# Optimization experiments

Measured on AMD Instinct MI355X. Metric: run time of the kernel, lower is better.

The kernel has to match this reference:

```python
import jax, jax.numpy as jnp
import numpy as np

N_NODES = 100000
N_EDGES = 1600000
D_IN, D_HID, D_OUT = 128, 64, 64


def setup_inputs() -> dict:
    key = jax.random.key(0)
    k0, k1, k2, k3 = jax.random.split(key, 4)
    X = jax.random.normal(k0, (N_NODES, D_IN), dtype=jnp.float32)
    E = jax.random.randint(k1, (2, N_EDGES), 0, N_NODES, dtype=jnp.int32)
    W1 = jax.random.normal(k2, (D_IN, D_HID), dtype=jnp.float32) * 0.05
    b1 = jnp.zeros((D_HID,), dtype=jnp.float32)
    W2 = jax.random.normal(k3, (D_HID, D_OUT), dtype=jnp.float32) * 0.05
    b2 = jnp.zeros((D_OUT,), dtype=jnp.float32)
    return {"V": N_NODES, "E": E, "X": X, "W1": W1, "b1": b1, "W2": W2, "b2": b2}


def _gcn_layer(X, W, b, src, dst, norm, n):
    # GCNConv: linear transform (no bias), gather, degree-normalize, scatter-add, + bias
    Xl = X @ W                              # [n, d_out]
    msg = Xl[src] * norm[:, None]           # [n_edges_sl, d_out] gather
    out = jax.ops.segment_sum(msg, dst, num_segments=n)  # scatter-add
    return out + b


def reference(V, E, X, W1, b1, W2, b2):
    n = X.shape[0]
    # add self loops (add_self_loops=True)
    loop = jnp.arange(n, dtype=E.dtype)
    src = jnp.concatenate([E[0], loop])
    dst = jnp.concatenate([E[1], loop])
    # symmetric gcn_norm: deg over target nodes (unit edge weights)
    deg = jax.ops.segment_sum(jnp.ones_like(dst, dtype=X.dtype), dst, num_segments=n)
    dinv = jnp.where(deg > 0, jax.lax.rsqrt(deg), 0.0)
    norm = dinv[src] * dinv[dst]
    H = jax.nn.relu(_gcn_layer(X, W1, b1, src, dst, norm, n))
    # last layer: no ReLU (matches torch module)
    return _gcn_layer(H, W2, b2, src, dst, norm, n)
```

## Files before the change

### kernel.cpp

```cpp
#include <hip/hip_runtime.h>

#define NT 256
#define TILE 256
#define TILE_SH 8
#define BSTRIDE 8192
#define BSTRIDE_SH 13
#define EPB 4096
#define ITB 16
#define NBUCK_PAD 512

static inline int cdiv(long long a, long long b) { return (int)((a + b - 1) / b); }

typedef unsigned int uint32;
typedef unsigned short ushort16;
typedef short bf16x8 __attribute__((ext_vector_type(8)));
typedef float f32x4 __attribute__((ext_vector_type(4)));

__device__ __forceinline__ ushort16 f2bf(float f) {
  uint32 u = __float_as_uint(f);
  u = (u + 0x7FFF + ((u >> 16) & 1)) >> 16;
  return (ushort16)u;
}
__device__ __forceinline__ float bflo(uint32 w) { return __uint_as_float(w << 16); }
__device__ __forceinline__ float bfhi(uint32 w) { return __uint_as_float(w & 0xFFFF0000u); }
__device__ __forceinline__ float bf2f(ushort16 h) { return __uint_as_float(((uint32)h) << 16); }

template <int K, int BFIN, int SPLIT>
__device__ __forceinline__ void gemm_body(const void* __restrict__ Xp,
                                          const float* __restrict__ W,
                                          uint2* __restrict__ Yb, int n, int base,
                                          unsigned short* Xh, unsigned short* XlA,
                                          unsigned short* Wt) {
  constexpr int STR = K + 8;
  const int tid = threadIdx.x;

  for (int i = tid; i < K * 64; i += NT) {
    int k = i >> 6, nn = i & 63;
    Wt[nn * STR + k] = f2bf(W[i]);
  }
  if (BFIN) {
    constexpr int NU = K / 8;
    const uint4* X4 = (const uint4*)Xp;
    for (int i = tid; i < 64 * NU; i += NT) {
      int row = i / NU, u = i % NU;
      int v = base + row;
      uint4 val = make_uint4(0u, 0u, 0u, 0u);
      if (v < n) val = X4[(size_t)v * NU + u];
      *(uint4*)&Xh[row * STR + u * 8] = val;
    }
  } else {
    constexpr int KQ = K / 4;
    const float4* X4 = (const float4*)Xp;
    for (int i = tid; i < 64 * KQ; i += NT) {
      int row = i / KQ, q = i % KQ;
      int v = base + row;
      float4 val = make_float4(0.f, 0.f, 0.f, 0.f);
      if (v < n) val = X4[(size_t)v * KQ + q];
      ushort16 h0 = f2bf(val.x), h1 = f2bf(val.y), h2 = f2bf(val.z), h3 = f2bf(val.w);
      uint2 hh;
      hh.x = (uint32)h0 | ((uint32)h1 << 16);
      hh.y = (uint32)h2 | ((uint32)h3 << 16);
      *(uint2*)&Xh[row * STR + q * 4] = hh;
      if (SPLIT) {
        ushort16 l0 = f2bf(val.x - bf2f(h0)), l1 = f2bf(val.y - bf2f(h1));
        ushort16 l2 = f2bf(val.z - bf2f(h2)), l3 = f2bf(val.w - bf2f(h3));
        uint2 ll;
        ll.x = (uint32)l0 | ((uint32)l1 << 16);
        ll.y = (uint32)l2 | ((uint32)l3 << 16);
        *(uint2*)&XlA[row * STR + q * 4] = ll;
      }
    }
  }
  __syncthreads();

  const int w = tid >> 6;
  const int lane = tid & 63;
  const int r = lane & 15;
  const int quad = lane >> 4;
  const int rloc = w * 16 + r;

  f32x4 acc[4];
#pragma unroll
  for (int i = 0; i < 4; ++i) acc[i] = (f32x4)(0.f);

#pragma unroll
  for (int ks = 0; ks < K / 32; ++ks) {
    const int koff = ks * 32 + quad * 8;
    bf16x8 xh = *(const bf16x8*)&Xh[rloc * STR + koff];
    bf16x8 xl;
    if (SPLIT) xl = *(const bf16x8*)&XlA[rloc * STR + koff];
#pragma unroll
    for (int nt = 0; nt < 4; ++nt) {
      bf16x8 wf = *(const bf16x8*)&Wt[(nt * 16 + r) * STR + koff];
      if (SPLIT)
        acc[nt] = __builtin_amdgcn_mfma_f32_16x16x32_bf16(wf, xl, acc[nt], 0, 0, 0);
      acc[nt] = __builtin_amdgcn_mfma_f32_16x16x32_bf16(wf, xh, acc[nt], 0, 0, 0);
    }
  }

  int v = base + rloc;
  if (v < n) {
#pragma unroll
    for (int nt = 0; nt < 4; ++nt) {
      uint2 u;
      u.x = (uint32)f2bf(acc[nt][0]) | ((uint32)f2bf(acc[nt][1]) << 16);
      u.y = (uint32)f2bf(acc[nt][2]) | ((uint32)f2bf(acc[nt][3]) << 16);
      Yb[(size_t)v * 16 + nt * 4 + quad] = u;
    }
  }
}

struct GemmSh {
  unsigned short Xh[64 * 136];
  unsigned short Xl[64 * 136];
  unsigned short Wt[64 * 136];
};
struct ScatSh {
  int cnt[NBUCK_PAD];
  int lcur[NBUCK_PAD];
  int delta[NBUCK_PAD];
  int hs[NT];
  uint32 sorted[EPB];
  unsigned short bid[EPB];
};
union FusedSh {
  GemmSh g;
  ScatSh s;
};

__global__ __launch_bounds__(NT) void k_fused(const int* __restrict__ src,
                                              const int* __restrict__ dst,
                                              int* __restrict__ bcursor,
                                              uint32* __restrict__ buck, int nE,
                                              int nbuck, int gscat,
                                              const float* __restrict__ X,
                                              const float* __restrict__ W1,
                                              uint2* __restrict__ Yb, int n) {
  __shared__ FusedSh sm;
  if ((int)blockIdx.x >= gscat) {
    gemm_body<128, 0, 1>(X, W1, Yb, n, ((int)blockIdx.x - gscat) * 64, sm.g.Xh,
                         sm.g.Xl, sm.g.Wt);
    return;
  }
  const int t = threadIdx.x;
  for (int i = t; i < NBUCK_PAD; i += NT) sm.s.cnt[i] = 0;
  __syncthreads();
  const int e0 = blockIdx.x * EPB;
  const int ne = min(EPB, nE - e0);
#pragma unroll
  for (int it = 0; it < ITB; ++it) {
    int e = e0 + it * NT + t;
    if (e < nE) atomicAdd(&sm.s.cnt[dst[e] >> TILE_SH], 1);
  }
  __syncthreads();
  int c0 = sm.s.cnt[2 * t], c1 = sm.s.cnt[2 * t + 1];
  int ps = c0 + c1;
  sm.s.hs[t] = ps;
  __syncthreads();
  for (int o = 1; o < NT; o <<= 1) {
    int x = (t >= o) ? sm.s.hs[t - o] : 0;
    __syncthreads();
    sm.s.hs[t] += x;
    __syncthreads();
  }
  int lb0 = sm.s.hs[t] - ps;
  int lb1 = lb0 + c0;
  sm.s.lcur[2 * t] = lb0;
  sm.s.lcur[2 * t + 1] = lb1;
  {
    int b0 = 2 * t, b1 = 2 * t + 1;
    if (b0 < nbuck) {
      int g0 = c0 ? atomicAdd(&bcursor[b0], c0) : 0;
      sm.s.delta[b0] = (b0 << BSTRIDE_SH) + g0 - lb0;
    }
    if (b1 < nbuck) {
      int g1 = c1 ? atomicAdd(&bcursor[b1], c1) : 0;
      sm.s.delta[b1] = (b1 << BSTRIDE_SH) + g1 - lb1;
    }
  }
  __syncthreads();
#pragma unroll
  for (int it = 0; it < ITB; ++it) {
    int e = e0 + it * NT + t;
    if (e < nE) {
      int d = dst[e];
      int b = d >> TILE_SH;
      int p = atomicAdd(&sm.s.lcur[b], 1);
      sm.s.sorted[p] = (uint32)src[e] | ((uint32)(d & (TILE - 1)) << 24);
      sm.s.bid[p] = (unsigned short)b;
    }
  }
  __syncthreads();
  for (int i = t; i < ne; i += NT) {
    int b = sm.s.bid[i];
    int g = sm.s.delta[b] + i;
    if (g < ((b + 1) << BSTRIDE_SH))
      buck[g] = sm.s.sorted[i];
  }
}

__global__ __launch_bounds__(NT) void k_bcsr(const uint32* __restrict__ buck,
                                             const int* __restrict__ bcursor,
                                             int2* __restrict__ rowspan,
                                             float* __restrict__ dinv,
                                             int* __restrict__ srcs, int n) {
  __shared__ int hist[TILE];
  __shared__ int hs[NT];
  __shared__ int off[TILE];
  __shared__ uint32 sarr[BSTRIDE];
  const int b = blockIdx.x;
  const int t = threadIdx.x;
  const int W = b * BSTRIDE;
  const int cntb = min(bcursor[b], BSTRIDE);
  const int v0 = b << TILE_SH;
  const int nv = min(TILE, n - v0);
  hist[t] = 0;
  __syncthreads();
  for (int i = t; i < cntb; i += NT) atomicAdd(&hist[buck[W + i] >> 24], 1);
  __syncthreads();
  int h = hist[t];
  hs[t] = h;
  __syncthreads();
  for (int o = 1; o < NT; o <<= 1) {
    int x = (t >= o) ? hs[t - o] : 0;
    __syncthreads();
    hs[t] += x;
    __syncthreads();
  }
  int ex = hs[t] - h;
  off[t] = ex;
  if (t < nv) {
    rowspan[v0 + t] = make_int2(W + ex, W + ex + h);
    dinv[v0 + t] = rsqrtf((float)(h + 1));
  }
  __syncthreads();
  for (int i = t; i < cntb; i += NT) {
    uint32 w = buck[W + i];
    int ld = (int)(w >> 24);
    int p = atomicAdd(&off[ld], 1);
    sarr[p] = w & 0x00FFFFFFu;
  }
  __syncthreads();
  for (int i = t; i < cntb; i += NT) srcs[W + i] = (int)sarr[i];
}

struct Acc8 {
  float a0, a1, a2, a3, a4, a5, a6, a7;
  __device__ __forceinline__ void madd(uint4 r, float s) {
    a0 = fmaf(bflo(r.x), s, a0); a1 = fmaf(bfhi(r.x), s, a1);
    a2 = fmaf(bflo(r.y), s, a2); a3 = fmaf(bfhi(r.y), s, a3);
    a4 = fmaf(bflo(r.z), s, a4); a5 = fmaf(bfhi(r.z), s, a5);
    a6 = fmaf(bflo(r.w), s, a6); a7 = fmaf(bfhi(r.w), s, a7);
  }
};

template <int RELU, int OUTBF>
__global__ __launch_bounds__(NT) void k_gather(const int2* __restrict__ rowspan,
                                               const int* __restrict__ srcs,
                                               const float* __restrict__ dinv,
                                               const uint4* __restrict__ Xn,
                                               const float* __restrict__ bias,
                                               void* __restrict__ outp, int n) {
  const int gt = blockIdx.x * NT + threadIdx.x;
  const int lane = threadIdx.x & 63;
  const int v = ((gt >> 6) << 1) + (lane >> 5);
  if (v >= n) return;
  const int l5 = lane & 31;
  const int part = l5 & 7;
  const int q = l5 >> 3;
  const int2 rs = rowspan[v];
  const int beg = rs.x, end = rs.y;
  const float dv = dinv[v];
  Acc8 A = {0.f, 0.f, 0.f, 0.f, 0.f, 0.f, 0.f, 0.f};
  int j = beg + q;
  for (; j + 4 < end; j += 8) {
    int s0 = srcs[j];
    int s1 = srcs[j + 4];
    float ds0 = dinv[s0];
    float ds1 = dinv[s1];
    uint4 r0 = Xn[(size_t)s0 * 8 + part];
    uint4 r1 = Xn[(size_t)s1 * 8 + part];
    A.madd(r0, ds0);
    A.madd(r1, ds1);
  }
  if (j < end) {
    int s = srcs[j];
    A.madd(Xn[(size_t)s * 8 + part], dinv[s]);
  }
#pragma unroll
  for (int m = 8; m <= 16; m <<= 1) {
    A.a0 += __shfl_xor(A.a0, m);
    A.a1 += __shfl_xor(A.a1, m);
    A.a2 += __shfl_xor(A.a2, m);
    A.a3 += __shfl_xor(A.a3, m);
    A.a4 += __shfl_xor(A.a4, m);
    A.a5 += __shfl_xor(A.a5, m);
    A.a6 += __shfl_xor(A.a6, m);
    A.a7 += __shfl_xor(A.a7, m);
  }
  if (q == 0) {
    uint4 wv = Xn[(size_t)v * 8 + part];
    const float4* b4 = (const float4*)bias;
    float4 b0 = b4[part * 2], b1 = b4[part * 2 + 1];
    float r0 = dv * (A.a0 + dv * bflo(wv.x)) + b0.x;
    float r1 = dv * (A.a1 + dv * bfhi(wv.x)) + b0.y;
    float r2 = dv * (A.a2 + dv * bflo(wv.y)) + b0.z;
    float r3 = dv * (A.a3 + dv * bfhi(wv.y)) + b0.w;
    float r4 = dv * (A.a4 + dv * bflo(wv.z)) + b1.x;
    float r5 = dv * (A.a5 + dv * bfhi(wv.z)) + b1.y;
    float r6 = dv * (A.a6 + dv * bflo(wv.w)) + b1.z;
    float r7 = dv * (A.a7 + dv * bfhi(wv.w)) + b1.w;
    if (RELU) {
      r0 = fmaxf(r0, 0.f); r1 = fmaxf(r1, 0.f); r2 = fmaxf(r2, 0.f); r3 = fmaxf(r3, 0.f);
      r4 = fmaxf(r4, 0.f); r5 = fmaxf(r5, 0.f); r6 = fmaxf(r6, 0.f); r7 = fmaxf(r7, 0.f);
    }
    if (OUTBF) {
      uint4 u;
      u.x = (uint32)f2bf(r0) | ((uint32)f2bf(r1) << 16);
      u.y = (uint32)f2bf(r2) | ((uint32)f2bf(r3) << 16);
      u.z = (uint32)f2bf(r4) | ((uint32)f2bf(r5) << 16);
      u.w = (uint32)f2bf(r6) | ((uint32)f2bf(r7) << 16);
      ((uint4*)outp)[(size_t)v * 8 + part] = u;
    } else {
      float4* o4 = (float4*)outp;
      o4[(size_t)v * 16 + part * 2] = make_float4(r0, r1, r2, r3);
      o4[(size_t)v * 16 + part * 2 + 1] = make_float4(r4, r5, r6, r7);
    }
  }
}

__global__ __launch_bounds__(NT) void k_gemm2(const void* __restrict__ Xp,
                                              const float* __restrict__ W,
                                              uint2* __restrict__ Yb, int n) {
  __shared__ unsigned short Xh[64 * 72];
  __shared__ unsigned short Wt[64 * 72];
  gemm_body<64, 1, 0>(Xp, W, Yb, n, blockIdx.x * 64, Xh, Xh , Wt);
}

extern "C" void kernel_launch(void* const* d_in, const int* in_sizes, int n_in,
                              void* d_out, int out_size, void* d_ws, size_t ws_size,
                              hipStream_t stream) {
  const int* E = (const int*)d_in[1];
  const float* X = (const float*)d_in[2];
  const float* W1 = (const float*)d_in[3];
  const float* b1 = (const float*)d_in[4];
  const float* W2 = (const float*)d_in[5];
  const float* b2 = (const float*)d_in[6];
  float* out = (float*)d_out;

  const int n = in_sizes[2] / 128;
  const int nE = in_sizes[1] / 2;
  const int* src = E;
  const int* dst = E + nE;
  const int nbuck = cdiv(n, TILE);

  char* ws = (char*)d_ws;
  size_t off = 0;
  auto alloc = [&](size_t bytes) {
    size_t o = off;
    off = (off + bytes + 255) & ~(size_t)255;
    return (void*)(ws + o);
  };
  int2* rowspan = (int2*)alloc((size_t)n * 8);
  float* dinv = (float*)alloc((size_t)n * 4);
  int* bcursor = (int*)alloc((size_t)nbuck * 4);
  uint32* buck = (uint32*)alloc((size_t)nbuck * BSTRIDE * 4);
  int* srcs = (int*)alloc((size_t)nbuck * BSTRIDE * 4);
  uint2* Xn = (uint2*)alloc((size_t)n * 64 * 2);
  uint2* H = (uint2*)alloc((size_t)n * 64 * 2);

  const int gscat = cdiv(nE, EPB);
  const int ggemm = cdiv(n, 64);
  const int gthreads_blocks = cdiv((long long)n * 32, NT);

  hipMemsetAsync(bcursor, 0, (size_t)nbuck * 4, stream);

  k_fused<<<gscat + ggemm, NT, 0, stream>>>(src, dst, bcursor, buck, nE, nbuck,
                                            gscat, X, W1, Xn, n);
  k_bcsr<<<nbuck, NT, 0, stream>>>(buck, bcursor, rowspan, dinv, srcs, n);

  k_gather<1, 1><<<gthreads_blocks, NT, 0, stream>>>(rowspan, srcs, dinv,
                                                     (const uint4*)Xn, b1, H, n);

  k_gemm2<<<cdiv(n, 64), NT, 0, stream>>>(H, W2, Xn, n);
  k_gather<0, 0><<<gthreads_blocks, NT, 0, stream>>>(rowspan, srcs, dinv,
                                                     (const uint4*)Xn, b2, out, n);
}
```

Before: 244.9 us.

## Use persistent GEMM blocks that stage W once and load X straight to registers

The GEMM blocks in the fused scatter kernel and in k_gemm2 become persistent grid-stride loops over 64-row tiles. Each block converts W to bf16 in shared memory once and reuses it across its tiles. X fragments are now loaded directly from global memory into MFMA operand registers instead of being staged through LDS, which frees shared memory and removes a sync per tile. The scatter path also keeps its dst values in registers so they are not loaded twice. The trade-offs are fixed grid sizes (1024 blocks), launch-bounds hints, and direct global loads that are less coalesced.

```diff
diff --git a/kernel.cpp b/kernel.cpp
--- a/kernel.cpp
+++ b/kernel.cpp
@@ -25,80 +25,85 @@
 __device__ __forceinline__ float bfhi(uint32 w) { return __uint_as_float(w & 0xFFFF0000u); }
 __device__ __forceinline__ float bf2f(ushort16 h) { return __uint_as_float(((uint32)h) << 16); }
 
+template <int K>
+__device__ __forceinline__ void stage_W(const float* __restrict__ W,
+                                        unsigned short* __restrict__ Wt) {
+  constexpr int STR = K + 8;
+  for (int i = threadIdx.x; i < K * 64; i += NT) {
+    int k = i >> 6, nn = i & 63;
+    Wt[nn * STR + k] = f2bf(W[i]);
+  }
+}
+
 template <int K, int BFIN, int SPLIT>
-__device__ __forceinline__ void gemm_body(const void* __restrict__ Xp,
-                                          const float* __restrict__ W,
-                                          uint2* __restrict__ Yb, int n, int base,
-                                          unsigned short* Xh, unsigned short* XlA,
-                                          unsigned short* Wt) {
+__device__ __forceinline__ void gemm_tile(const void* __restrict__ Xp,
+                                          const unsigned short* __restrict__ Wt,
+                                          uint2* __restrict__ Yb, int n, int base) {
   constexpr int STR = K + 8;
   const int tid = threadIdx.x;
-
-  for (int i = tid; i < K * 64; i += NT) {
-    int k = i >> 6, nn = i & 63;
-    Wt[nn * STR + k] = f2bf(W[i]);
-  }
-  if (BFIN) {
-    constexpr int NU = K / 8;
-    const uint4* X4 = (const uint4*)Xp;
-    for (int i = tid; i < 64 * NU; i += NT) {
-      int row = i / NU, u = i % NU;
-      int v = base + row;
-      uint4 val = make_uint4(0u, 0u, 0u, 0u);
-      if (v < n) val = X4[(size_t)v * NU + u];
-      *(uint4*)&Xh[row * STR + u * 8] = val;
-    }
-  } else {
-    constexpr int KQ = K / 4;
-    const float4* X4 = (const float4*)Xp;
-    for (int i = tid; i < 64 * KQ; i += NT) {
-      int row = i / KQ, q = i % KQ;
-      int v = base + row;
-      float4 val = make_float4(0.f, 0.f, 0.f, 0.f);
-      if (v < n) val = X4[(size_t)v * KQ + q];
-      ushort16 h0 = f2bf(val.x), h1 = f2bf(val.y), h2 = f2bf(val.z), h3 = f2bf(val.w);
-      uint2 hh;
-      hh.x = (uint32)h0 | ((uint32)h1 << 16);
-      hh.y = (uint32)h2 | ((uint32)h3 << 16);
-      *(uint2*)&Xh[row * STR + q * 4] = hh;
-      if (SPLIT) {
-        ushort16 l0 = f2bf(val.x - bf2f(h0)), l1 = f2bf(val.y - bf2f(h1));
-        ushort16 l2 = f2bf(val.z - bf2f(h2)), l3 = f2bf(val.w - bf2f(h3));
-        uint2 ll;
-        ll.x = (uint32)l0 | ((uint32)l1 << 16);
-        ll.y = (uint32)l2 | ((uint32)l3 << 16);
-        *(uint2*)&XlA[row * STR + q * 4] = ll;
-      }
-    }
-  }
-  __syncthreads();
-
   const int w = tid >> 6;
   const int lane = tid & 63;
   const int r = lane & 15;
   const int quad = lane >> 4;
   const int rloc = w * 16 + r;
+  const int v = base + rloc;
 
   f32x4 acc[4];
 #pragma unroll
   for (int i = 0; i < 4; ++i) acc[i] = (f32x4)(0.f);
 
-#pragma unroll
-  for (int ks = 0; ks < K / 32; ++ks) {
-    const int koff = ks * 32 + quad * 8;
-    bf16x8 xh = *(const bf16x8*)&Xh[rloc * STR + koff];
-    bf16x8 xl;
-    if (SPLIT) xl = *(const bf16x8*)&XlA[rloc * STR + koff];
-#pragma unroll
-    for (int nt = 0; nt < 4; ++nt) {
-      bf16x8 wf = *(const bf16x8*)&Wt[(nt * 16 + r) * STR + koff];
-      if (SPLIT)
-        acc[nt] = __builtin_amdgcn_mfma_f32_16x16x32_bf16(wf, xl, acc[nt], 0, 0, 0);
-      acc[nt] = __builtin_amdgcn_mfma_f32_16x16x32_bf16(wf, xh, acc[nt], 0, 0, 0);
-    }
-  }
-
-  int v = base + rloc;
+  if (BFIN) {
+    const uint4* X4 = (const uint4*)Xp;
+    bf16x8 xf[K / 32];
+#pragma unroll
+    for (int ks = 0; ks < K / 32; ++ks) {
+      uint4 u = make_uint4(0u, 0u, 0u, 0u);
+      if (v < n) u = X4[(size_t)v * (K / 8) + ks * 4 + quad];
+      xf[ks] = *(const bf16x8*)&u;
+    }
+#pragma unroll
+    for (int ks = 0; ks < K / 32; ++ks) {
+      const int koff = ks * 32 + quad * 8;
+#pragma unroll
+      for (int nt = 0; nt < 4; ++nt) {
+        bf16x8 wf = *(const bf16x8*)&Wt[(nt * 16 + r) * STR + koff];
+        acc[nt] = __builtin_amdgcn_mfma_f32_16x16x32_bf16(wf, xf[ks], acc[nt], 0, 0, 0);
+      }
+    }
+  } else {
+    const float4* X4 = (const float4*)Xp;
+    float4 a[K / 32][2];
+#pragma unroll
+    for (int ks = 0; ks < K / 32; ++ks) {
+      a[ks][0] = make_float4(0.f, 0.f, 0.f, 0.f);
+      a[ks][1] = make_float4(0.f, 0.f, 0.f, 0.f);
+      if (v < n) {
+        a[ks][0] = X4[(size_t)v * (K / 4) + ks * 8 + quad * 2];
+        a[ks][1] = X4[(size_t)v * (K / 4) + ks * 8 + quad * 2 + 1];
+      }
+    }
+#pragma unroll
+    for (int ks = 0; ks < K / 32; ++ks) {
+      float f[8] = {a[ks][0].x, a[ks][0].y, a[ks][0].z, a[ks][0].w,
+                    a[ks][1].x, a[ks][1].y, a[ks][1].z, a[ks][1].w};
+      bf16x8 xh, xl;
+#pragma unroll
+      for (int j = 0; j < 8; ++j) {
+        ushort16 h = f2bf(f[j]);
+        xh[j] = (short)h;
+        if (SPLIT) xl[j] = (short)f2bf(f[j] - bf2f(h));
+      }
+      const int koff = ks * 32 + quad * 8;
+#pragma unroll
+      for (int nt = 0; nt < 4; ++nt) {
+        bf16x8 wf = *(const bf16x8*)&Wt[(nt * 16 + r) * STR + koff];
+        if (SPLIT)
+          acc[nt] = __builtin_amdgcn_mfma_f32_16x16x32_bf16(wf, xl, acc[nt], 0, 0, 0);
+        acc[nt] = __builtin_amdgcn_mfma_f32_16x16x32_bf16(wf, xh, acc[nt], 0, 0, 0);
+      }
+    }
+  }
+
   if (v < n) {
 #pragma unroll
     for (int nt = 0; nt < 4; ++nt) {
@@ -110,11 +115,6 @@
   }
 }
 
-struct GemmSh {
-  unsigned short Xh[64 * 136];
-  unsigned short Xl[64 * 136];
-  unsigned short Wt[64 * 136];
-};
 struct ScatSh {
   int cnt[NBUCK_PAD];
   int lcur[NBUCK_PAD];
@@ -124,22 +124,21 @@
   unsigned short bid[EPB];
 };
 union FusedSh {
-  GemmSh g;
+  unsigned short wt[64 * 136];
   ScatSh s;
 };
 
-__global__ __launch_bounds__(NT) void k_fused(const int* __restrict__ src,
-                                              const int* __restrict__ dst,
-                                              int* __restrict__ bcursor,
-                                              uint32* __restrict__ buck, int nE,
-                                              int nbuck, int gscat,
-                                              const float* __restrict__ X,
-                                              const float* __restrict__ W1,
-                                              uint2* __restrict__ Yb, int n) {
+__global__ __launch_bounds__(NT, 4) void k_fused(
+    const int* __restrict__ src, const int* __restrict__ dst,
+    int* __restrict__ bcursor, uint32* __restrict__ buck, int nE, int nbuck,
+    int gscat, int ggemm, int ntile, const float* __restrict__ X,
+    const float* __restrict__ W1, uint2* __restrict__ Yb, int n) {
   __shared__ FusedSh sm;
   if ((int)blockIdx.x >= gscat) {
-    gemm_body<128, 0, 1>(X, W1, Yb, n, ((int)blockIdx.x - gscat) * 64, sm.g.Xh,
-                         sm.g.Xl, sm.g.Wt);
+    stage_W<128>(W1, sm.wt);
+    __syncthreads();
+    for (int tile = (int)blockIdx.x - gscat; tile < ntile; tile += ggemm)
+      gemm_tile<128, 0, 1>(X, sm.wt, Yb, n, tile * 64);
     return;
   }
   const int t = threadIdx.x;
@@ -147,10 +146,12 @@
   __syncthreads();
   const int e0 = blockIdx.x * EPB;
   const int ne = min(EPB, nE - e0);
+  int dreg[ITB];
 #pragma unroll
   for (int it = 0; it < ITB; ++it) {
     int e = e0 + it * NT + t;
-    if (e < nE) atomicAdd(&sm.s.cnt[dst[e] >> TILE_SH], 1);
+    dreg[it] = (e < nE) ? dst[e] : -1;
+    if (dreg[it] >= 0) atomicAdd(&sm.s.cnt[dreg[it] >> TILE_SH], 1);
   }
   __syncthreads();
   int c0 = sm.s.cnt[2 * t], c1 = sm.s.cnt[2 * t + 1];
@@ -182,8 +183,8 @@
 #pragma unroll
   for (int it = 0; it < ITB; ++it) {
     int e = e0 + it * NT + t;
-    if (e < nE) {
-      int d = dst[e];
+    if (dreg[it] >= 0) {
+      int d = dreg[it];
       int b = d >> TILE_SH;
       int p = atomicAdd(&sm.s.lcur[b], 1);
       sm.s.sorted[p] = (uint32)src[e] | ((uint32)(d & (TILE - 1)) << 24);
@@ -329,12 +330,15 @@
   }
 }
 
-__global__ __launch_bounds__(NT) void k_gemm2(const void* __restrict__ Xp,
-                                              const float* __restrict__ W,
-                                              uint2* __restrict__ Yb, int n) {
-  __shared__ unsigned short Xh[64 * 72];
+__global__ __launch_bounds__(NT, 4) void k_gemm2(const void* __restrict__ Xp,
+                                                 const float* __restrict__ W,
+                                                 uint2* __restrict__ Yb, int n,
+                                                 int gg, int ntile) {
   __shared__ unsigned short Wt[64 * 72];
-  gemm_body<64, 1, 0>(Xp, W, Yb, n, blockIdx.x * 64, Xh, Xh , Wt);
+  stage_W<64>(W, Wt);
+  __syncthreads();
+  for (int tile = (int)blockIdx.x; tile < ntile; tile += gg)
+    gemm_tile<64, 1, 0>(Xp, Wt, Yb, n, tile * 64);
 }
 
 extern "C" void kernel_launch(void* const* d_in, const int* in_sizes, int n_in,
@@ -370,19 +374,20 @@
   uint2* H = (uint2*)alloc((size_t)n * 64 * 2);
 
   const int gscat = cdiv(nE, EPB);
-  const int ggemm = cdiv(n, 64);
+  const int ntile = cdiv(n, 64);
+  const int ggemm = 1024 - gscat;
   const int gthreads_blocks = cdiv((long long)n * 32, NT);
 
   hipMemsetAsync(bcursor, 0, (size_t)nbuck * 4, stream);
 
   k_fused<<<gscat + ggemm, NT, 0, stream>>>(src, dst, bcursor, buck, nE, nbuck,
-                                            gscat, X, W1, Xn, n);
+                                            gscat, ggemm, ntile, X, W1, Xn, n);
   k_bcsr<<<nbuck, NT, 0, stream>>>(buck, bcursor, rowspan, dinv, srcs, n);
 
   k_gather<1, 1><<<gthreads_blocks, NT, 0, stream>>>(rowspan, srcs, dinv,
                                                      (const uint4*)Xn, b1, H, n);
 
-  k_gemm2<<<cdiv(n, 64), NT, 0, stream>>>(H, W2, Xn, n);
+  k_gemm2<<<1024, NT, 0, stream>>>(H, W2, Xn, n, 1024, ntile);
   k_gather<0, 0><<<gthreads_blocks, NT, 0, stream>>>(rowspan, srcs, dinv,
                                                      (const uint4*)Xn, b2, out, n);
 }
```

Result: faster. 233.1 us (-4.8%).
